# Kernel optimization log

Measured on AMD Instinct MI355X. Metric: run time of the kernel, lower is better.

Reference implementation:

```python
import jax, jax.numpy as jnp
import numpy as np

N, F, E, B, D = 100000, 256, 128, 10000, 32
GAMMA, ZETA = -0.1, 1.1  # hard-concrete stretch params of L0Dense


def setup_inputs() -> dict:
    key = jax.random.key(0)
    ks = jax.random.split(key, 12)
    return {
        "nodes": jax.random.randint(ks[0], (B,), 0, N),
        "neigh_idx": jax.random.randint(ks[1], (B, D), 0, N),
        "neigh_mask": jax.random.bernoulli(ks[2], 0.9, (B, D)),
        "feature": jax.random.normal(ks[3], (N, F), jnp.float32),
        "W": jax.random.normal(ks[4], (F, E), jnp.float32) * 0.05,
        "b": jnp.zeros((E,), jnp.float32),
        "qz_loga": jax.random.normal(ks[5], (F,), jnp.float32),
        "att1_w": jax.random.normal(ks[6], (2 * E, E), jnp.float32) * 0.05,
        "att1_b": jnp.zeros((E,), jnp.float32),
        "att2_w": jax.random.normal(ks[7], (E, E), jnp.float32) * 0.05,
        "att2_b": jnp.zeros((E,), jnp.float32),
        "att3_w": jax.random.normal(ks[8], (E, 1), jnp.float32) * 0.05,
        "att3_b": jnp.zeros((1,), jnp.float32),
    }


def reference(nodes, neigh_idx, neigh_mask, feature, W, b, qz_loga,
              att1_w, att1_b, att2_w, att2_b, att3_w, att3_b):
    # L0Dense, deterministic (eval) hard-concrete gate on input dims
    z = jnp.clip(jax.nn.sigmoid(qz_loga) * (ZETA - GAMMA) + GAMMA, 0.0, 1.0)
    We = W * z[:, None]                                  # [F, E]

    node_feat = feature[nodes] @ We + b                   # [B, E]
    neigh_feat = feature[neigh_idx] @ We + b              # [B, D, E]

    # GraphRec-style attention MLP over (neighbor, center) pairs
    h = jnp.concatenate(
        [neigh_feat, jnp.broadcast_to(node_feat[:, None, :], neigh_feat.shape)],
        axis=-1)                                          # [B, D, 2E]
    h = jax.nn.relu(h @ att1_w + att1_b)
    h = jax.nn.relu(h @ att2_w + att2_b)
    scores = (h @ att3_w + att3_b)[..., 0]                # [B, D]
    scores = jnp.where(neigh_mask, scores, -1e30)
    att = jax.nn.softmax(scores, axis=-1)                 # [B, D]

    agg = jnp.einsum('bd,bde->be', att, neigh_feat)       # weighted sum
    has_neigh = neigh_mask.any(axis=-1, keepdims=True)
    return jnp.where(has_neigh, agg, node_feat)           # n==0 fallback
```

## Files before the change

kernel.cpp:

```cpp
#include <hip/hip_runtime.h>
#include <hip/hip_bf16.h>
#include <math.h>

#define NN 100000
#define FF 256
#define EE 128
#define BB_ 10000
#define DD 32

typedef __attribute__((ext_vector_type(8))) short short8;
typedef __attribute__((ext_vector_type(4))) float f32x4;

__device__ __forceinline__ short f2bf(float f) {
  __hip_bfloat16 h = __float2bfloat16(f);
  union { __hip_bfloat16 h; short s; } u; u.h = h;
  return u.s;
}
__device__ __forceinline__ float bf2f(short s) {
  union { unsigned u; float f; } v;
  v.u = ((unsigned)(unsigned short)s) << 16;
  return v.f;
}

__device__ __forceinline__ void gll16(const float* g, float* lds) {
  __builtin_amdgcn_global_load_lds(
      (const __attribute__((address_space(1))) unsigned int*)g,
      (__attribute__((address_space(3))) unsigned int*)lds, 16, 0, 0);
}

__global__ __launch_bounds__(256) void k_prep(
    const float* __restrict__ W, const float* __restrict__ qz,
    const float* __restrict__ a1w, const float* __restrict__ a2w,
    const float* __restrict__ bb,
    float* __restrict__ Wef32, short* __restrict__ BT2,
    short* __restrict__ a1wTc, short* __restrict__ w2T,
    float* __restrict__ bias2) {
  int i = blockIdx.x * 256 + threadIdx.x;
  if (i < 32768) {
    int f = i >> 7, e = i & 127;
    float g = qz[f];
    float s = 1.0f / (1.0f + expf(-g));
    float z = fminf(fmaxf(s * 1.2f - 0.1f, 0.0f), 1.0f);
    float v = W[f * 128 + e] * z;
    Wef32[f * 128 + e] = v;
    BT2[e * 256 + f] = f2bf(v);
  } else if (i < 49152) {
    int t = i - 32768; int n = t >> 7, k = t & 127;
    a1wTc[n * 128 + k] = f2bf(a1w[(128 + k) * 128 + n]);
  } else if (i < 65536) {
    int t = i - 49152; int n = t >> 7, k = t & 127;
    w2T[n * 128 + k] = f2bf(a2w[k * 128 + n]);
  } else if (i < 65664) {
    bias2[i - 65536] = bb[i - 65536];
  }
}

__global__ __launch_bounds__(256) void k_compose(
    const float* __restrict__ Wef32, const float* __restrict__ a1w,
    const float* __restrict__ a1b, const float* __restrict__ bb,
    short* __restrict__ BT2, float* __restrict__ bias2) {
  const int n = blockIdx.x;
  const int f = threadIdx.x;
  float s = 0.f;
  for (int e = 0; e < 128; ++e)
    s = fmaf(a1w[e * 128 + n], Wef32[f * 128 + e], s);
  BT2[(size_t)(128 + n) * 256 + f] = f2bf(s);
  if (f == 0) {
    float by = a1b[n];
    for (int e = 0; e < 128; ++e) by = fmaf(bb[e], a1w[e * 128 + n], by);
    bias2[128 + n] = by;
  }
}

__global__ __launch_bounds__(256) void k_xy(
    const float* __restrict__ feat, const short* __restrict__ BT2,
    const float* __restrict__ bias2, short* __restrict__ XY, int M) {
  __shared__ float As[2][32 * 256];
  const int tid = threadIdx.x;
  const int wave = tid >> 6, lane = tid & 63;
  const int wn = wave;
  const int l15 = lane & 15, lg = lane >> 4;
  const int NT = M >> 5;
  const int G = gridDim.x;

  short8 bfr[8][4];
#pragma unroll
  for (int ks = 0; ks < 8; ++ks)
#pragma unroll
    for (int j = 0; j < 4; ++j)
      bfr[ks][j] = *(const short8*)(BT2 +
          (size_t)(wn * 64 + j * 16 + l15) * 256 + (ks * 4 + lg) * 8);
  float bv4[4];
#pragma unroll
  for (int j = 0; j < 4; ++j) bv4[j] = bias2[wn * 64 + j * 16 + l15];

  int t = blockIdx.x;
  if (t < NT) {
#pragma unroll
    for (int it = 0; it < 8; ++it) {
      int r = it * 4 + wave;
      gll16(feat + (size_t)(t * 32 + r) * 256 + ((lane ^ (r & 7)) * 4),
            &As[0][r * 256]);
    }
  }

  int cur = 0;
  for (; t < NT; t += G) {
    const int tn = t + G;
    __builtin_amdgcn_s_barrier();
    if (tn < NT) {
#pragma unroll
      for (int it = 0; it < 8; ++it) {
        int r = it * 4 + wave;
        gll16(feat + (size_t)(tn * 32 + r) * 256 + ((lane ^ (r & 7)) * 4),
              &As[cur ^ 1][r * 256]);
      }
      asm volatile("s_waitcnt vmcnt(8)" ::: "memory");
    } else {
      asm volatile("s_waitcnt vmcnt(0)" ::: "memory");
    }
    __builtin_amdgcn_s_barrier();
    __builtin_amdgcn_sched_barrier(0);

    f32x4 acc[2][4];
#pragma unroll
    for (int i = 0; i < 2; ++i)
#pragma unroll
      for (int j = 0; j < 4; ++j) acc[i][j] = (f32x4){0.f, 0.f, 0.f, 0.f};

    const float* Ab = &As[cur][0];
#pragma unroll
    for (int ks = 0; ks < 8; ++ks) {
      const int kg = ks * 4 + lg;
#pragma unroll
      for (int i = 0; i < 2; ++i) {
        const int r = i * 16 + l15;
        const int sw = r & 7;
        const int c0 = (2 * kg) ^ sw;
        const int c1 = (2 * kg + 1) ^ sw;
        float4 flo = *(const float4*)(Ab + r * 256 + c0 * 4);
        float4 fhi = *(const float4*)(Ab + r * 256 + c1 * 4);
        short8 af;
        af[0] = f2bf(flo.x); af[1] = f2bf(flo.y);
        af[2] = f2bf(flo.z); af[3] = f2bf(flo.w);
        af[4] = f2bf(fhi.x); af[5] = f2bf(fhi.y);
        af[6] = f2bf(fhi.z); af[7] = f2bf(fhi.w);
        __builtin_amdgcn_s_setprio(1);
#pragma unroll
        for (int j = 0; j < 4; ++j)
          acc[i][j] = __builtin_amdgcn_mfma_f32_16x16x32_bf16(
              af, bfr[ks][j], acc[i][j], 0, 0, 0);
        __builtin_amdgcn_s_setprio(0);
      }
    }

#pragma unroll
    for (int i = 0; i < 2; ++i) {
#pragma unroll
      for (int r = 0; r < 4; ++r) {
        int row = t * 32 + i * 16 + lg * 4 + r;
#pragma unroll
        for (int j = 0; j < 4; ++j) {
          int col = wn * 64 + j * 16 + l15;
          XY[(size_t)row * 256 + col] = f2bf(acc[i][j][r] + bv4[j]);
        }
      }
    }
    cur ^= 1;
  }
}

template <int K, int LDA, int LDC, bool AF32, bool OUTBF16>
__global__ __launch_bounds__(256) void k_mm(
    const void* __restrict__ Ap, const short* __restrict__ BT,
    const float* __restrict__ bias, const int* __restrict__ idx,
    void* __restrict__ Cp, int M) {
  __shared__ short As[128 * 64];
  __shared__ short Bs[128 * 64];
  const int tid = threadIdx.x;
  const int mb = blockIdx.x * 128;
  const int col0 = blockIdx.y * 128;
  const int wave = tid >> 6, lane = tid & 63;
  const int wr = wave >> 1, wc = wave & 1;
  const int l15 = lane & 15, lg = lane >> 4;

  size_t abase[4];
#pragma unroll
  for (int s = 0; s < 4; ++s) {
    int row = (tid + s * 256) >> 3;
    int grow = mb + row;
    int gr = 0;
    if (grow < M) gr = idx ? idx[grow] : grow;
    abase[s] = (size_t)gr * LDA;
  }

  f32x4 acc[4][4];
#pragma unroll
  for (int i = 0; i < 4; ++i)
#pragma unroll
    for (int j = 0; j < 4; ++j) acc[i][j] = (f32x4){0.f, 0.f, 0.f, 0.f};

  for (int k0 = 0; k0 < K; k0 += 64) {
#pragma unroll
    for (int s = 0; s < 4; ++s) {
      int q = tid + s * 256;
      int row = q >> 3, c = q & 7;
      short8 av;
      if (AF32) {
        const float* ap = (const float*)Ap + abase[s] + k0 + c * 8;
        float4 f0 = *(const float4*)ap;
        float4 f1 = *(const float4*)(ap + 4);
        av[0] = f2bf(f0.x); av[1] = f2bf(f0.y);
        av[2] = f2bf(f0.z); av[3] = f2bf(f0.w);
        av[4] = f2bf(f1.x); av[5] = f2bf(f1.y);
        av[6] = f2bf(f1.z); av[7] = f2bf(f1.w);
      } else {
        av = *(const short8*)((const short*)Ap + abase[s] + k0 + c * 8);
      }
      *(short8*)(As + row * 64 + 8 * (c ^ (row & 7))) = av;
      short8 bv = *(const short8*)(BT + (size_t)(col0 + row) * K + k0 + c * 8);
      *(short8*)(Bs + row * 64 + 8 * (c ^ (row & 7))) = bv;
    }
    __syncthreads();
#pragma unroll
    for (int ks = 0; ks < 2; ++ks) {
      int c = ks * 4 + lg;
      short8 af[4], bfv[4];
#pragma unroll
      for (int i = 0; i < 4; ++i) {
        int r = wr * 64 + i * 16 + l15;
        af[i] = *(short8*)(As + r * 64 + 8 * (c ^ (r & 7)));
        int n = wc * 64 + i * 16 + l15;
        bfv[i] = *(short8*)(Bs + n * 64 + 8 * (c ^ (n & 7)));
      }
#pragma unroll
      for (int i = 0; i < 4; ++i)
#pragma unroll
        for (int j = 0; j < 4; ++j)
          acc[i][j] = __builtin_amdgcn_mfma_f32_16x16x32_bf16(
              af[i], bfv[j], acc[i][j], 0, 0, 0);
    }
    __syncthreads();
  }

  float bv4[4];
#pragma unroll
  for (int j = 0; j < 4; ++j) {
    int col = wc * 64 + j * 16 + l15;
    bv4[j] = bias ? bias[col0 + col] : 0.f;
  }
#pragma unroll
  for (int i = 0; i < 4; ++i) {
#pragma unroll
    for (int r = 0; r < 4; ++r) {
      int row = mb + wr * 64 + i * 16 + lg * 4 + r;
      if (row < M) {
#pragma unroll
        for (int j = 0; j < 4; ++j) {
          int col = wc * 64 + j * 16 + l15;
          float v = acc[i][j][r] + bv4[j];
          if (OUTBF16)
            ((short*)Cp)[(size_t)row * LDC + col0 + col] = f2bf(v);
          else
            ((float*)Cp)[(size_t)row * LDC + col0 + col] = v;
        }
      }
    }
  }
}

__global__ __launch_bounds__(256) void k_attn5(
    const short* __restrict__ XY, const float* __restrict__ P,
    const int* __restrict__ nodes, const int* __restrict__ nidx,
    const int* __restrict__ nmask, const short* __restrict__ w2T,
    const float* __restrict__ b2, const float* __restrict__ w3,
    const float* __restrict__ b3, float* __restrict__ out) {
  __shared__ short xs[4][32 * 128];
  __shared__ float sc_s[4][32];
  __shared__ float att_s[4][32];
  const int tid = threadIdx.x;
  const int wave = tid >> 6, lane = tid & 63;
  const int b = blockIdx.x * 4 + wave;
  const int l15 = lane & 15, lg = lane >> 4;
  const int* nb = nidx + b * DD;

  const int m = nmask[(size_t)b * DD + (lane & 31)];

  short8 xtmp[8];
#pragma unroll
  for (int it = 0; it < 8; ++it)
    xtmp[it] = *(const short8*)(XY + (size_t)nb[it * 4 + lg] * 256 + l15 * 8);
  const int nid0 = nb[l15];
  const int nid1 = nb[16 + l15];
  const short* yr0 = XY + (size_t)nid0 * 256 + 128;
  const short* yr1 = XY + (size_t)nid1 * 256 + 128;
  short8 y0v[4], y1v[4];
#pragma unroll
  for (int ks = 0; ks < 4; ++ks) {
    const int k0 = ks * 32 + lg * 8;
    y0v[ks] = *(const short8*)(yr0 + k0);
    y1v[ks] = *(const short8*)(yr1 + k0);
  }
  const float* pr = P + (size_t)b * EE;
  float4 pv[8];
#pragma unroll
  for (int q = 0; q < 4; ++q) {
    const int k0 = q * 32 + lg * 8;
    pv[2 * q] = *(const float4*)(pr + k0);
    pv[2 * q + 1] = *(const float4*)(pr + k0 + 4);
  }

#pragma unroll
  for (int it = 0; it < 8; ++it)
    *(short8*)&xs[wave][(it * 4 + lg) * 128 + l15 * 8] = xtmp[it];

  short8 a0[4], a1[4];
#pragma unroll
  for (int ks = 0; ks < 4; ++ks) {
    float pf[8] = {pv[2 * ks].x, pv[2 * ks].y, pv[2 * ks].z, pv[2 * ks].w,
                   pv[2 * ks + 1].x, pv[2 * ks + 1].y, pv[2 * ks + 1].z,
                   pv[2 * ks + 1].w};
#pragma unroll
    for (int e = 0; e < 8; ++e) {
      a0[ks][e] = f2bf(fmaxf(bf2f(y0v[ks][e]) + pf[e], 0.f));
      a1[ks][e] = f2bf(fmaxf(bf2f(y1v[ks][e]) + pf[e], 0.f));
    }
  }

  float sp[2][4];
#pragma unroll
  for (int i = 0; i < 2; ++i)
#pragma unroll
    for (int r = 0; r < 4; ++r) sp[i][r] = 0.f;

#pragma unroll
  for (int cg = 0; cg < 2; ++cg) {
    f32x4 acc[2][4];
#pragma unroll
    for (int i = 0; i < 2; ++i)
#pragma unroll
      for (int j = 0; j < 4; ++j) acc[i][j] = (f32x4){0.f, 0.f, 0.f, 0.f};
#pragma unroll
    for (int ks = 0; ks < 4; ++ks) {
      const int k0 = ks * 32 + lg * 8;
      short8 bfv[4];
#pragma unroll
      for (int j = 0; j < 4; ++j)
        bfv[j] = *(const short8*)(w2T +
            (size_t)(cg * 64 + j * 16 + l15) * EE + k0);
      __builtin_amdgcn_s_setprio(1);
#pragma unroll
      for (int j = 0; j < 4; ++j) {
        acc[0][j] = __builtin_amdgcn_mfma_f32_16x16x32_bf16(a0[ks], bfv[j],
                                                            acc[0][j], 0, 0, 0);
        acc[1][j] = __builtin_amdgcn_mfma_f32_16x16x32_bf16(a1[ks], bfv[j],
                                                            acc[1][j], 0, 0, 0);
      }
      __builtin_amdgcn_s_setprio(0);
    }
#pragma unroll
    for (int j = 0; j < 4; ++j) {
      const int col = cg * 64 + j * 16 + l15;
      const float b2v = b2[col];
      const float w3v = w3[col];
#pragma unroll
      for (int i = 0; i < 2; ++i)
#pragma unroll
        for (int r = 0; r < 4; ++r)
          sp[i][r] += fmaxf(acc[i][j][r] + b2v, 0.f) * w3v;
    }
  }

#pragma unroll
  for (int off = 1; off <= 8; off <<= 1) {
#pragma unroll
    for (int i = 0; i < 2; ++i)
#pragma unroll
      for (int r = 0; r < 4; ++r) sp[i][r] += __shfl_xor(sp[i][r], off);
  }
  if (l15 == 0) {
#pragma unroll
    for (int i = 0; i < 2; ++i)
#pragma unroll
      for (int r = 0; r < 4; ++r)
        sc_s[wave][i * 16 + lg * 4 + r] = sp[i][r];
  }

  const int row = lane & 31;
  float s = sc_s[wave][row] + b3[0];
  if (!m) s = -1e30f;
  float mx = s;
#pragma unroll
  for (int off = 1; off <= 16; off <<= 1) mx = fmaxf(mx, __shfl_xor(mx, off));
  float e = expf(s - mx);
  float sum = e;
#pragma unroll
  for (int off = 1; off <= 16; off <<= 1) sum += __shfl_xor(sum, off);
  if (lane < 32) att_s[wave][row] = e / sum;
  const bool has = (__ballot(m != 0) != 0ull);

  float a0f = 0.f, a1f = 0.f;
  if (has) {
#pragma unroll
    for (int d = 0; d < 32; ++d) {
      const float a = att_s[wave][d];
      const unsigned xdw = *(const unsigned*)&xs[wave][d * 128 + 2 * lane];
      a0f += a * bf2f((short)(xdw & 0xffffu));
      a1f += a * bf2f((short)(xdw >> 16));
    }
  } else {
    const short* xr = XY + (size_t)nodes[b] * 256;
    unsigned x2 = *(const unsigned*)(xr + 2 * lane);
    a0f = bf2f((short)(x2 & 0xffffu));
    a1f = bf2f((short)(x2 >> 16));
  }
  *(float2*)(out + (size_t)b * EE + 2 * lane) = make_float2(a0f, a1f);
}

extern "C" void kernel_launch(void* const* d_in, const int* in_sizes, int n_in,
                              void* d_out, int out_size, void* d_ws,
                              size_t ws_size, hipStream_t stream) {
  const int* nodes = (const int*)d_in[0];
  const int* nidx = (const int*)d_in[1];
  const int* nmask = (const int*)d_in[2];
  const float* feature = (const float*)d_in[3];
  const float* W = (const float*)d_in[4];
  const float* bb = (const float*)d_in[5];
  const float* qz = (const float*)d_in[6];
  const float* a1w = (const float*)d_in[7];
  const float* a1b = (const float*)d_in[8];
  const float* a2w = (const float*)d_in[9];
  const float* a2b = (const float*)d_in[10];
  const float* a3w = (const float*)d_in[11];
  const float* a3b = (const float*)d_in[12];
  float* out = (float*)d_out;

  char* ws = (char*)d_ws;
  short* BT2   = (short*)(ws);
  float* Wef32 = (float*)(ws + 131072);
  short* a1wTc = (short*)(ws + 262144);
  short* w2T   = (short*)(ws + 294912);
  float* bias2 = (float*)(ws + 327680);
  short* XYb   = (short*)(ws + 524288);
  float* Pv    = (float*)(ws + 524288 + 51200000);

  k_prep<<<257, 256, 0, stream>>>(W, qz, a1w, a2w, bb, Wef32, BT2, a1wTc, w2T,
                                  bias2);
  k_compose<<<128, 256, 0, stream>>>(Wef32, a1w, a1b, bb, BT2, bias2);
  k_xy<<<512, 256, 0, stream>>>(feature, BT2, bias2, XYb, NN);
  k_mm<128, 256, 128, false, false><<<dim3((BB_ + 127) / 128, 1), 256, 0,
                                      stream>>>(XYb, a1wTc, nullptr, nodes, Pv,
                                                BB_);
  k_attn5<<<BB_ / 4, 256, 0, stream>>>(XYb, Pv, nodes, nidx, nmask, w2T, a2b,
                                       a3w, a3b, out);
}
```

Baseline: 125.0 us.

## Make attention kernel persistent with software-prefetched next batch item

The attention kernel now launches 625 blocks, and each wave processes 4 batch items strided by 2500. Indices, masks, the Y rows and P for the next item are prefetched while the current item's MFMAs run. The X rows for the weighted sum are loaded directly into registers instead of staged through LDS, and b2/w3 are hoisted out of the loop. This aims to hide gather latency, at the cost of higher register pressure (32 extra registers for xv) and fewer blocks to hide latency with.

Measured after the change: 123.0 us. Within noise of the previous version (-1.6%).

```diff
diff --git a/kernel.cpp b/kernel.cpp
--- a/kernel.cpp
+++ b/kernel.cpp
@@ -269,152 +269,178 @@
   }
 }
 
-__global__ __launch_bounds__(256) void k_attn5(
+__global__ __launch_bounds__(256) void k_attn6(
     const short* __restrict__ XY, const float* __restrict__ P,
     const int* __restrict__ nodes, const int* __restrict__ nidx,
     const int* __restrict__ nmask, const short* __restrict__ w2T,
     const float* __restrict__ b2, const float* __restrict__ w3,
     const float* __restrict__ b3, float* __restrict__ out) {
-  __shared__ short xs[4][32 * 128];
   __shared__ float sc_s[4][32];
   __shared__ float att_s[4][32];
   const int tid = threadIdx.x;
   const int wave = tid >> 6, lane = tid & 63;
-  const int b = blockIdx.x * 4 + wave;
   const int l15 = lane & 15, lg = lane >> 4;
-  const int* nb = nidx + b * DD;
-
-  const int m = nmask[(size_t)b * DD + (lane & 31)];
-
-  short8 xtmp[8];
-#pragma unroll
-  for (int it = 0; it < 8; ++it)
-    xtmp[it] = *(const short8*)(XY + (size_t)nb[it * 4 + lg] * 256 + l15 * 8);
-  const int nid0 = nb[l15];
-  const int nid1 = nb[16 + l15];
-  const short* yr0 = XY + (size_t)nid0 * 256 + 128;
-  const short* yr1 = XY + (size_t)nid1 * 256 + 128;
+  const int w0 = blockIdx.x * 4 + wave;
+  const float b3v = b3[0];
+
+  float b2v[2][4], w3v[2][4];
+#pragma unroll
+  for (int cg = 0; cg < 2; ++cg)
+#pragma unroll
+    for (int j = 0; j < 4; ++j) {
+      const int col = cg * 64 + j * 16 + l15;
+      b2v[cg][j] = b2[col];
+      w3v[cg][j] = w3[col];
+    }
+
+  int b = w0;
+  int xc = nidx[b * DD + (lane & 31)];
+  int mc = nmask[b * DD + (lane & 31)];
+  unsigned xfb = *(const unsigned*)(XY + (size_t)nodes[b] * 256 + 2 * lane);
+  int nb0 = __shfl(xc, l15), nb1 = __shfl(xc, 16 + l15);
   short8 y0v[4], y1v[4];
 #pragma unroll
   for (int ks = 0; ks < 4; ++ks) {
     const int k0 = ks * 32 + lg * 8;
-    y0v[ks] = *(const short8*)(yr0 + k0);
-    y1v[ks] = *(const short8*)(yr1 + k0);
-  }
-  const float* pr = P + (size_t)b * EE;
+    y0v[ks] = *(const short8*)(XY + (size_t)nb0 * 256 + 128 + k0);
+    y1v[ks] = *(const short8*)(XY + (size_t)nb1 * 256 + 128 + k0);
+  }
   float4 pv[8];
 #pragma unroll
   for (int q = 0; q < 4; ++q) {
     const int k0 = q * 32 + lg * 8;
-    pv[2 * q] = *(const float4*)(pr + k0);
-    pv[2 * q + 1] = *(const float4*)(pr + k0 + 4);
-  }
-
-#pragma unroll
-  for (int it = 0; it < 8; ++it)
-    *(short8*)&xs[wave][(it * 4 + lg) * 128 + l15 * 8] = xtmp[it];
-
-  short8 a0[4], a1[4];
-#pragma unroll
-  for (int ks = 0; ks < 4; ++ks) {
-    float pf[8] = {pv[2 * ks].x, pv[2 * ks].y, pv[2 * ks].z, pv[2 * ks].w,
-                   pv[2 * ks + 1].x, pv[2 * ks + 1].y, pv[2 * ks + 1].z,
-                   pv[2 * ks + 1].w};
-#pragma unroll
-    for (int e = 0; e < 8; ++e) {
-      a0[ks][e] = f2bf(fmaxf(bf2f(y0v[ks][e]) + pf[e], 0.f));
-      a1[ks][e] = f2bf(fmaxf(bf2f(y1v[ks][e]) + pf[e], 0.f));
-    }
-  }
-
-  float sp[2][4];
-#pragma unroll
-  for (int i = 0; i < 2; ++i)
-#pragma unroll
-    for (int r = 0; r < 4; ++r) sp[i][r] = 0.f;
-
-#pragma unroll
-  for (int cg = 0; cg < 2; ++cg) {
-    f32x4 acc[2][4];
+    pv[2 * q] = *(const float4*)(P + (size_t)b * EE + k0);
+    pv[2 * q + 1] = *(const float4*)(P + (size_t)b * EE + k0 + 4);
+  }
+
+#pragma unroll 1
+  for (int it = 0; it < 4; ++it) {
+    const int bn = (it < 3) ? b + 2500 : b;
+    int xn = nidx[bn * DD + (lane & 31)];
+    int mn = nmask[bn * DD + (lane & 31)];
+    unsigned xfbn =
+        *(const unsigned*)(XY + (size_t)nodes[bn] * 256 + 2 * lane);
+
+    unsigned xv[32];
+#pragma unroll
+    for (int d = 0; d < 32; ++d)
+      xv[d] = *(const unsigned*)(XY + (size_t)__shfl(xc, d) * 256 + 2 * lane);
+
+    short8 a0[4], a1[4];
+#pragma unroll
+    for (int ks = 0; ks < 4; ++ks) {
+      float pf[8] = {pv[2 * ks].x, pv[2 * ks].y, pv[2 * ks].z, pv[2 * ks].w,
+                     pv[2 * ks + 1].x, pv[2 * ks + 1].y, pv[2 * ks + 1].z,
+                     pv[2 * ks + 1].w};
+#pragma unroll
+      for (int e = 0; e < 8; ++e) {
+        a0[ks][e] = f2bf(fmaxf(bf2f(y0v[ks][e]) + pf[e], 0.f));
+        a1[ks][e] = f2bf(fmaxf(bf2f(y1v[ks][e]) + pf[e], 0.f));
+      }
+    }
+
+    float sp[2][4];
 #pragma unroll
     for (int i = 0; i < 2; ++i)
 #pragma unroll
-      for (int j = 0; j < 4; ++j) acc[i][j] = (f32x4){0.f, 0.f, 0.f, 0.f};
-#pragma unroll
-    for (int ks = 0; ks < 4; ++ks) {
-      const int k0 = ks * 32 + lg * 8;
-      short8 bfv[4];
-#pragma unroll
-      for (int j = 0; j < 4; ++j)
-        bfv[j] = *(const short8*)(w2T +
-            (size_t)(cg * 64 + j * 16 + l15) * EE + k0);
-      __builtin_amdgcn_s_setprio(1);
+      for (int r = 0; r < 4; ++r) sp[i][r] = 0.f;
+
+#pragma unroll
+    for (int cg = 0; cg < 2; ++cg) {
+      f32x4 acc[2][4];
+#pragma unroll
+      for (int i = 0; i < 2; ++i)
+#pragma unroll
+        for (int j = 0; j < 4; ++j) acc[i][j] = (f32x4){0.f, 0.f, 0.f, 0.f};
+#pragma unroll
+      for (int ks = 0; ks < 4; ++ks) {
+        const int k0 = ks * 32 + lg * 8;
+        short8 bfv[4];
+#pragma unroll
+        for (int j = 0; j < 4; ++j)
+          bfv[j] = *(const short8*)(w2T +
+              (size_t)(cg * 64 + j * 16 + l15) * EE + k0);
+        __builtin_amdgcn_s_setprio(1);
+#pragma unroll
+        for (int j = 0; j < 4; ++j) {
+          acc[0][j] = __builtin_amdgcn_mfma_f32_16x16x32_bf16(
+              a0[ks], bfv[j], acc[0][j], 0, 0, 0);
+          acc[1][j] = __builtin_amdgcn_mfma_f32_16x16x32_bf16(
+              a1[ks], bfv[j], acc[1][j], 0, 0, 0);
+        }
+        __builtin_amdgcn_s_setprio(0);
+      }
+      if (cg == 0) {
+        const int nb0n = __shfl(xn, l15), nb1n = __shfl(xn, 16 + l15);
+#pragma unroll
+        for (int ks = 0; ks < 4; ++ks) {
+          const int k0 = ks * 32 + lg * 8;
+          y0v[ks] = *(const short8*)(XY + (size_t)nb0n * 256 + 128 + k0);
+          y1v[ks] = *(const short8*)(XY + (size_t)nb1n * 256 + 128 + k0);
+        }
+      }
 #pragma unroll
       for (int j = 0; j < 4; ++j) {
-        acc[0][j] = __builtin_amdgcn_mfma_f32_16x16x32_bf16(a0[ks], bfv[j],
-                                                            acc[0][j], 0, 0, 0);
-        acc[1][j] = __builtin_amdgcn_mfma_f32_16x16x32_bf16(a1[ks], bfv[j],
-                                                            acc[1][j], 0, 0, 0);
-      }
-      __builtin_amdgcn_s_setprio(0);
-    }
-#pragma unroll
-    for (int j = 0; j < 4; ++j) {
-      const int col = cg * 64 + j * 16 + l15;
-      const float b2v = b2[col];
-      const float w3v = w3[col];
+#pragma unroll
+        for (int i = 0; i < 2; ++i)
+#pragma unroll
+          for (int r = 0; r < 4; ++r)
+            sp[i][r] += fmaxf(acc[i][j][r] + b2v[cg][j], 0.f) * w3v[cg][j];
+      }
+    }
+
+#pragma unroll
+    for (int q = 0; q < 4; ++q) {
+      const int k0 = q * 32 + lg * 8;
+      pv[2 * q] = *(const float4*)(P + (size_t)bn * EE + k0);
+      pv[2 * q + 1] = *(const float4*)(P + (size_t)bn * EE + k0 + 4);
+    }
+
+#pragma unroll
+    for (int off = 1; off <= 8; off <<= 1) {
 #pragma unroll
       for (int i = 0; i < 2; ++i)
 #pragma unroll
+        for (int r = 0; r < 4; ++r) sp[i][r] += __shfl_xor(sp[i][r], off);
+    }
+    if (l15 == 0) {
+#pragma unroll
+      for (int i = 0; i < 2; ++i)
+#pragma unroll
         for (int r = 0; r < 4; ++r)
-          sp[i][r] += fmaxf(acc[i][j][r] + b2v, 0.f) * w3v;
-    }
-  }
-
-#pragma unroll
-  for (int off = 1; off <= 8; off <<= 1) {
-#pragma unroll
-    for (int i = 0; i < 2; ++i)
-#pragma unroll
-      for (int r = 0; r < 4; ++r) sp[i][r] += __shfl_xor(sp[i][r], off);
-  }
-  if (l15 == 0) {
-#pragma unroll
-    for (int i = 0; i < 2; ++i)
-#pragma unroll
-      for (int r = 0; r < 4; ++r)
-        sc_s[wave][i * 16 + lg * 4 + r] = sp[i][r];
-  }
-
-  const int row = lane & 31;
-  float s = sc_s[wave][row] + b3[0];
-  if (!m) s = -1e30f;
-  float mx = s;
-#pragma unroll
-  for (int off = 1; off <= 16; off <<= 1) mx = fmaxf(mx, __shfl_xor(mx, off));
-  float e = expf(s - mx);
-  float sum = e;
-#pragma unroll
-  for (int off = 1; off <= 16; off <<= 1) sum += __shfl_xor(sum, off);
-  if (lane < 32) att_s[wave][row] = e / sum;
-  const bool has = (__ballot(m != 0) != 0ull);
-
-  float a0f = 0.f, a1f = 0.f;
-  if (has) {
-#pragma unroll
-    for (int d = 0; d < 32; ++d) {
-      const float a = att_s[wave][d];
-      const unsigned xdw = *(const unsigned*)&xs[wave][d * 128 + 2 * lane];
-      a0f += a * bf2f((short)(xdw & 0xffffu));
-      a1f += a * bf2f((short)(xdw >> 16));
-    }
-  } else {
-    const short* xr = XY + (size_t)nodes[b] * 256;
-    unsigned x2 = *(const unsigned*)(xr + 2 * lane);
-    a0f = bf2f((short)(x2 & 0xffffu));
-    a1f = bf2f((short)(x2 >> 16));
-  }
-  *(float2*)(out + (size_t)b * EE + 2 * lane) = make_float2(a0f, a1f);
+          sc_s[wave][i * 16 + lg * 4 + r] = sp[i][r];
+    }
+
+    const int row = lane & 31;
+    float s = sc_s[wave][row] + b3v;
+    if (!mc) s = -1e30f;
+    float mx = s;
+#pragma unroll
+    for (int off = 1; off <= 16; off <<= 1)
+      mx = fmaxf(mx, __shfl_xor(mx, off));
+    float e = expf(s - mx);
+    float sum = e;
+#pragma unroll
+    for (int off = 1; off <= 16; off <<= 1) sum += __shfl_xor(sum, off);
+    if (lane < 32) att_s[wave][row] = e / sum;
+    const bool has = (__ballot(mc != 0) != 0ull);
+
+    float a0f = 0.f, a1f = 0.f;
+    if (has) {
+#pragma unroll
+      for (int d = 0; d < 32; ++d) {
+        const float a = att_s[wave][d];
+        a0f += a * bf2f((short)(xv[d] & 0xffffu));
+        a1f += a * bf2f((short)(xv[d] >> 16));
+      }
+    } else {
+      a0f = bf2f((short)(xfb & 0xffffu));
+      a1f = bf2f((short)(xfb >> 16));
+    }
+    *(float2*)(out + (size_t)b * EE + 2 * lane) = make_float2(a0f, a1f);
+
+    xc = xn; mc = mn; xfb = xfbn; b = bn;
+  }
 }
 
 extern "C" void kernel_launch(void* const* d_in, const int* in_sizes, int n_in,
@@ -451,6 +477,6 @@
   k_mm<128, 256, 128, false, false><<<dim3((BB_ + 127) / 128, 1), 256, 0,
                                       stream>>>(XYb, a1wTc, nullptr, nodes, Pv,
                                                 BB_);
-  k_attn5<<<BB_ / 4, 256, 0, stream>>>(XYb, Pv, nodes, nidx, nmask, w2T, a2b,
-                                       a3w, a3b, out);
-}
+  k_attn6<<<625, 256, 0, stream>>>(XYb, Pv, nodes, nidx, nmask, w2T, a2b,
+                                   a3w, a3b, out);
+}
```

## Drop precomposed Y projection; compute neighbor attention layer-1 in the attention kernel

Applied to the files above, without the earlier changes.

The node-wide projection used to produce both X and a precomposed Y = X·att1_w_top for all 100k nodes, writing 256 bf16 values per node. Now it writes only X (128 columns), and the attention kernel runs the first attention layer with MFMA on the 32 gathered neighbor rows per center, staging the ReLU output in swizzled LDS. The k_compose launch and the fp32 Wef32 buffer are removed. The aim is to halve the big intermediate write and the gather traffic. The cost is extra MFMA work and LDS traffic inside the attention kernel, with the gathered X rows also held in registers.

After: 135.4 us. +8.3%, slower.

```diff
diff --git a/kernel.cpp b/kernel.cpp
--- a/kernel.cpp
+++ b/kernel.cpp
@@ -31,50 +31,30 @@
 __global__ __launch_bounds__(256) void k_prep(
     const float* __restrict__ W, const float* __restrict__ qz,
     const float* __restrict__ a1w, const float* __restrict__ a2w,
-    const float* __restrict__ bb,
-    float* __restrict__ Wef32, short* __restrict__ BT2,
-    short* __restrict__ a1wTc, short* __restrict__ w2T,
-    float* __restrict__ bias2) {
+    short* __restrict__ BT2, short* __restrict__ a1wTn,
+    short* __restrict__ a1wTc, short* __restrict__ w2T) {
   int i = blockIdx.x * 256 + threadIdx.x;
   if (i < 32768) {
     int f = i >> 7, e = i & 127;
     float g = qz[f];
     float s = 1.0f / (1.0f + expf(-g));
     float z = fminf(fmaxf(s * 1.2f - 0.1f, 0.0f), 1.0f);
-    float v = W[f * 128 + e] * z;
-    Wef32[f * 128 + e] = v;
-    BT2[e * 256 + f] = f2bf(v);
+    BT2[e * 256 + f] = f2bf(W[f * 128 + e] * z);
   } else if (i < 49152) {
-    int t = i - 32768; int n = t >> 7, k = t & 127;
-    a1wTc[n * 128 + k] = f2bf(a1w[(128 + k) * 128 + n]);
+    int t = i - 32768; int c = t >> 7, f = t & 127;
+    a1wTn[c * 128 + f] = f2bf(a1w[f * 128 + c]);
   } else if (i < 65536) {
     int t = i - 49152; int n = t >> 7, k = t & 127;
+    a1wTc[n * 128 + k] = f2bf(a1w[(128 + k) * 128 + n]);
+  } else if (i < 81920) {
+    int t = i - 65536; int n = t >> 7, k = t & 127;
     w2T[n * 128 + k] = f2bf(a2w[k * 128 + n]);
-  } else if (i < 65664) {
-    bias2[i - 65536] = bb[i - 65536];
-  }
-}
-
-__global__ __launch_bounds__(256) void k_compose(
-    const float* __restrict__ Wef32, const float* __restrict__ a1w,
-    const float* __restrict__ a1b, const float* __restrict__ bb,
-    short* __restrict__ BT2, float* __restrict__ bias2) {
-  const int n = blockIdx.x;
-  const int f = threadIdx.x;
-  float s = 0.f;
-  for (int e = 0; e < 128; ++e)
-    s = fmaf(a1w[e * 128 + n], Wef32[f * 128 + e], s);
-  BT2[(size_t)(128 + n) * 256 + f] = f2bf(s);
-  if (f == 0) {
-    float by = a1b[n];
-    for (int e = 0; e < 128; ++e) by = fmaf(bb[e], a1w[e * 128 + n], by);
-    bias2[128 + n] = by;
   }
 }
 
 __global__ __launch_bounds__(256) void k_xy(
     const float* __restrict__ feat, const short* __restrict__ BT2,
-    const float* __restrict__ bias2, short* __restrict__ XY, int M) {
+    const float* __restrict__ bb, short* __restrict__ X, int M) {
   __shared__ float As[2][32 * 256];
   const int tid = threadIdx.x;
   const int wave = tid >> 6, lane = tid & 63;
@@ -83,16 +63,16 @@
   const int NT = M >> 5;
   const int G = gridDim.x;
 
-  short8 bfr[8][4];
+  short8 bfr[8][2];
 #pragma unroll
   for (int ks = 0; ks < 8; ++ks)
 #pragma unroll
-    for (int j = 0; j < 4; ++j)
+    for (int j = 0; j < 2; ++j)
       bfr[ks][j] = *(const short8*)(BT2 +
-          (size_t)(wn * 64 + j * 16 + l15) * 256 + (ks * 4 + lg) * 8);
-  float bv4[4];
-#pragma unroll
-  for (int j = 0; j < 4; ++j) bv4[j] = bias2[wn * 64 + j * 16 + l15];
+          (size_t)(wn * 32 + j * 16 + l15) * 256 + (ks * 4 + lg) * 8);
+  float bv2[2];
+#pragma unroll
+  for (int j = 0; j < 2; ++j) bv2[j] = bb[wn * 32 + j * 16 + l15];
 
   int t = blockIdx.x;
   if (t < NT) {
@@ -122,11 +102,11 @@
     __builtin_amdgcn_s_barrier();
     __builtin_amdgcn_sched_barrier(0);
 
-    f32x4 acc[2][4];
+    f32x4 acc[2][2];
 #pragma unroll
     for (int i = 0; i < 2; ++i)
 #pragma unroll
-      for (int j = 0; j < 4; ++j) acc[i][j] = (f32x4){0.f, 0.f, 0.f, 0.f};
+      for (int j = 0; j < 2; ++j) acc[i][j] = (f32x4){0.f, 0.f, 0.f, 0.f};
 
     const float* Ab = &As[cur][0];
 #pragma unroll
@@ -147,7 +127,7 @@
         af[6] = f2bf(fhi.z); af[7] = f2bf(fhi.w);
         __builtin_amdgcn_s_setprio(1);
 #pragma unroll
-        for (int j = 0; j < 4; ++j)
+        for (int j = 0; j < 2; ++j)
           acc[i][j] = __builtin_amdgcn_mfma_f32_16x16x32_bf16(
               af, bfr[ks][j], acc[i][j], 0, 0, 0);
         __builtin_amdgcn_s_setprio(0);
@@ -160,9 +140,9 @@
       for (int r = 0; r < 4; ++r) {
         int row = t * 32 + i * 16 + lg * 4 + r;
 #pragma unroll
-        for (int j = 0; j < 4; ++j) {
-          int col = wn * 64 + j * 16 + l15;
-          XY[(size_t)row * 256 + col] = f2bf(acc[i][j][r] + bv4[j]);
+        for (int j = 0; j < 2; ++j) {
+          int col = wn * 32 + j * 16 + l15;
+          X[(size_t)row * EE + col] = f2bf(acc[i][j][r] + bv2[j]);
         }
       }
     }
@@ -170,16 +150,14 @@
   }
 }
 
-template <int K, int LDA, int LDC, bool AF32, bool OUTBF16>
 __global__ __launch_bounds__(256) void k_mm(
-    const void* __restrict__ Ap, const short* __restrict__ BT,
+    const short* __restrict__ Ap, const short* __restrict__ BT,
     const float* __restrict__ bias, const int* __restrict__ idx,
-    void* __restrict__ Cp, int M) {
+    float* __restrict__ Cp, int M) {
   __shared__ short As[128 * 64];
   __shared__ short Bs[128 * 64];
   const int tid = threadIdx.x;
   const int mb = blockIdx.x * 128;
-  const int col0 = blockIdx.y * 128;
   const int wave = tid >> 6, lane = tid & 63;
   const int wr = wave >> 1, wc = wave & 1;
   const int l15 = lane & 15, lg = lane >> 4;
@@ -190,8 +168,8 @@
     int row = (tid + s * 256) >> 3;
     int grow = mb + row;
     int gr = 0;
-    if (grow < M) gr = idx ? idx[grow] : grow;
-    abase[s] = (size_t)gr * LDA;
+    if (grow < M) gr = idx[grow];
+    abase[s] = (size_t)gr * EE;
   }
 
   f32x4 acc[4][4];
@@ -200,25 +178,14 @@
 #pragma unroll
     for (int j = 0; j < 4; ++j) acc[i][j] = (f32x4){0.f, 0.f, 0.f, 0.f};
 
-  for (int k0 = 0; k0 < K; k0 += 64) {
+  for (int k0 = 0; k0 < 128; k0 += 64) {
 #pragma unroll
     for (int s = 0; s < 4; ++s) {
       int q = tid + s * 256;
       int row = q >> 3, c = q & 7;
-      short8 av;
-      if (AF32) {
-        const float* ap = (const float*)Ap + abase[s] + k0 + c * 8;
-        float4 f0 = *(const float4*)ap;
-        float4 f1 = *(const float4*)(ap + 4);
-        av[0] = f2bf(f0.x); av[1] = f2bf(f0.y);
-        av[2] = f2bf(f0.z); av[3] = f2bf(f0.w);
-        av[4] = f2bf(f1.x); av[5] = f2bf(f1.y);
-        av[6] = f2bf(f1.z); av[7] = f2bf(f1.w);
-      } else {
-        av = *(const short8*)((const short*)Ap + abase[s] + k0 + c * 8);
-      }
+      short8 av = *(const short8*)(Ap + abase[s] + k0 + c * 8);
       *(short8*)(As + row * 64 + 8 * (c ^ (row & 7))) = av;
-      short8 bv = *(const short8*)(BT + (size_t)(col0 + row) * K + k0 + c * 8);
+      short8 bv = *(const short8*)(BT + (size_t)row * 128 + k0 + c * 8);
       *(short8*)(Bs + row * 64 + 8 * (c ^ (row & 7))) = bv;
     }
     __syncthreads();
@@ -245,10 +212,7 @@
 
   float bv4[4];
 #pragma unroll
-  for (int j = 0; j < 4; ++j) {
-    int col = wc * 64 + j * 16 + l15;
-    bv4[j] = bias ? bias[col0 + col] : 0.f;
-  }
+  for (int j = 0; j < 4; ++j) bv4[j] = bias[wc * 64 + j * 16 + l15];
 #pragma unroll
   for (int i = 0; i < 4; ++i) {
 #pragma unroll
@@ -258,91 +222,108 @@
 #pragma unroll
         for (int j = 0; j < 4; ++j) {
           int col = wc * 64 + j * 16 + l15;
-          float v = acc[i][j][r] + bv4[j];
-          if (OUTBF16)
-            ((short*)Cp)[(size_t)row * LDC + col0 + col] = f2bf(v);
-          else
-            ((float*)Cp)[(size_t)row * LDC + col0 + col] = v;
+          Cp[(size_t)row * EE + col] = acc[i][j][r] + bv4[j];
         }
       }
     }
   }
 }
 
-__global__ __launch_bounds__(256) void k_attn5(
-    const short* __restrict__ XY, const float* __restrict__ P,
+__global__ __launch_bounds__(256) void k_attn9(
+    const short* __restrict__ Xb, const float* __restrict__ P,
     const int* __restrict__ nodes, const int* __restrict__ nidx,
-    const int* __restrict__ nmask, const short* __restrict__ w2T,
-    const float* __restrict__ b2, const float* __restrict__ w3,
-    const float* __restrict__ b3, float* __restrict__ out) {
-  __shared__ short xs[4][32 * 128];
+    const int* __restrict__ nmask, const short* __restrict__ a1nT,
+    const short* __restrict__ w2T, const float* __restrict__ b2,
+    const float* __restrict__ w3, const float* __restrict__ b3,
+    float* __restrict__ out) {
+  __shared__ short h1s[4][32 * 128];
   __shared__ float sc_s[4][32];
   __shared__ float att_s[4][32];
   const int tid = threadIdx.x;
   const int wave = tid >> 6, lane = tid & 63;
+  const int l15 = lane & 15, lg = lane >> 4;
+  const int dl = lane & 31;
   const int b = blockIdx.x * 4 + wave;
-  const int l15 = lane & 15, lg = lane >> 4;
-  const int* nb = nidx + b * DD;
-
-  const int m = nmask[(size_t)b * DD + (lane & 31)];
-
-  short8 xtmp[8];
-#pragma unroll
-  for (int it = 0; it < 8; ++it)
-    xtmp[it] = *(const short8*)(XY + (size_t)nb[it * 4 + lg] * 256 + l15 * 8);
-  const int nid0 = nb[l15];
-  const int nid1 = nb[16 + l15];
-  const short* yr0 = XY + (size_t)nid0 * 256 + 128;
-  const short* yr1 = XY + (size_t)nid1 * 256 + 128;
-  short8 y0v[4], y1v[4];
+
+  const int ni = nidx[b * DD + dl];
+  const int m = nmask[b * DD + dl];
+  const int r0 = __shfl(ni, l15);
+  const int r1 = __shfl(ni, 16 + l15);
+
+  short8 xa0[4], xa1[4];
 #pragma unroll
   for (int ks = 0; ks < 4; ++ks) {
     const int k0 = ks * 32 + lg * 8;
-    y0v[ks] = *(const short8*)(yr0 + k0);
-    y1v[ks] = *(const short8*)(yr1 + k0);
-  }
-  const float* pr = P + (size_t)b * EE;
-  float4 pv[8];
-#pragma unroll
-  for (int q = 0; q < 4; ++q) {
-    const int k0 = q * 32 + lg * 8;
-    pv[2 * q] = *(const float4*)(pr + k0);
-    pv[2 * q + 1] = *(const float4*)(pr + k0 + 4);
-  }
-
-#pragma unroll
-  for (int it = 0; it < 8; ++it)
-    *(short8*)&xs[wave][(it * 4 + lg) * 128 + l15 * 8] = xtmp[it];
-
-  short8 a0[4], a1[4];
-#pragma unroll
-  for (int ks = 0; ks < 4; ++ks) {
-    float pf[8] = {pv[2 * ks].x, pv[2 * ks].y, pv[2 * ks].z, pv[2 * ks].w,
-                   pv[2 * ks + 1].x, pv[2 * ks + 1].y, pv[2 * ks + 1].z,
-                   pv[2 * ks + 1].w};
-#pragma unroll
-    for (int e = 0; e < 8; ++e) {
-      a0[ks][e] = f2bf(fmaxf(bf2f(y0v[ks][e]) + pf[e], 0.f));
-      a1[ks][e] = f2bf(fmaxf(bf2f(y1v[ks][e]) + pf[e], 0.f));
-    }
-  }
-
-  float sp[2][4];
-#pragma unroll
-  for (int i = 0; i < 2; ++i)
-#pragma unroll
-    for (int r = 0; r < 4; ++r) sp[i][r] = 0.f;
+    xa0[ks] = *(const short8*)(Xb + (size_t)r0 * EE + k0);
+    xa1[ks] = *(const short8*)(Xb + (size_t)r1 * EE + k0);
+  }
+  unsigned xv[32];
+#pragma unroll
+  for (int d = 0; d < 32; ++d)
+    xv[d] = *(const unsigned*)(Xb + (size_t)__shfl(ni, d) * EE + 2 * lane);
 
 #pragma unroll
   for (int cg = 0; cg < 2; ++cg) {
-    f32x4 acc[2][4];
+    f32x4 a1[2][4];
 #pragma unroll
     for (int i = 0; i < 2; ++i)
 #pragma unroll
-      for (int j = 0; j < 4; ++j) acc[i][j] = (f32x4){0.f, 0.f, 0.f, 0.f};
+      for (int j = 0; j < 4; ++j) a1[i][j] = (f32x4){0.f, 0.f, 0.f, 0.f};
 #pragma unroll
     for (int ks = 0; ks < 4; ++ks) {
       const int k0 = ks * 32 + lg * 8;
+      short8 bfv[4];
+#pragma unroll
+      for (int j = 0; j < 4; ++j)
+        bfv[j] = *(const short8*)(a1nT +
+            (size_t)(cg * 64 + j * 16 + l15) * EE + k0);
+      __builtin_amdgcn_s_setprio(1);
+#pragma unroll
+      for (int j = 0; j < 4; ++j) {
+        a1[0][j] = __builtin_amdgcn_mfma_f32_16x16x32_bf16(xa0[ks], bfv[j],
+                                                           a1[0][j], 0, 0, 0);
+        a1[1][j] = __builtin_amdgcn_mfma_f32_16x16x32_bf16(xa1[ks], bfv[j],
+                                                           a1[1][j], 0, 0, 0);
+      }
+      __builtin_amdgcn_s_setprio(0);
+    }
+#pragma unroll
+    for (int j = 0; j < 4; ++j) {
+      const int col = cg * 64 + j * 16 + l15;
+      const float pj = P[(size_t)b * EE + col];
+      const int cc = col >> 3;
+      const int ce = col & 7;
+#pragma unroll
+      for (int i = 0; i < 2; ++i)
+#pragma unroll
+        for (int r = 0; r < 4; ++r) {
+          const int row = i * 16 + lg * 4 + r;
+          h1s[wave][row * 128 + 8 * (cc ^ (row & 7)) + ce] =
+              f2bf(fmaxf(a1[i][j][r] + pj, 0.f));
+        }
+    }
+  }
+
+  float sp[2][4];
+#pragma unroll
+  for (int i = 0; i < 2; ++i)
+#pragma unroll
+    for (int r = 0; r < 4; ++r) sp[i][r] = 0.f;
+
+#pragma unroll
+  for (int cg = 0; cg < 2; ++cg) {
+    f32x4 a2[2][4];
+#pragma unroll
+    for (int i = 0; i < 2; ++i)
+#pragma unroll
+      for (int j = 0; j < 4; ++j) a2[i][j] = (f32x4){0.f, 0.f, 0.f, 0.f};
+#pragma unroll
+    for (int ks = 0; ks < 4; ++ks) {
+      const int k0 = ks * 32 + lg * 8;
+      const int c = ks * 4 + lg;
+      short8 af0 = *(short8*)&h1s[wave][l15 * 128 + 8 * (c ^ (l15 & 7))];
+      short8 af1 =
+          *(short8*)&h1s[wave][(16 + l15) * 128 + 8 * (c ^ (l15 & 7))];
       short8 bfv[4];
 #pragma unroll
       for (int j = 0; j < 4; ++j)
@@ -351,10 +332,10 @@
       __builtin_amdgcn_s_setprio(1);
 #pragma unroll
       for (int j = 0; j < 4; ++j) {
-        acc[0][j] = __builtin_amdgcn_mfma_f32_16x16x32_bf16(a0[ks], bfv[j],
-                                                            acc[0][j], 0, 0, 0);
-        acc[1][j] = __builtin_amdgcn_mfma_f32_16x16x32_bf16(a1[ks], bfv[j],
-                                                            acc[1][j], 0, 0, 0);
+        a2[0][j] = __builtin_amdgcn_mfma_f32_16x16x32_bf16(af0, bfv[j],
+                                                           a2[0][j], 0, 0, 0);
+        a2[1][j] = __builtin_amdgcn_mfma_f32_16x16x32_bf16(af1, bfv[j],
+                                                           a2[1][j], 0, 0, 0);
       }
       __builtin_amdgcn_s_setprio(0);
     }
@@ -367,7 +348,7 @@
       for (int i = 0; i < 2; ++i)
 #pragma unroll
         for (int r = 0; r < 4; ++r)
-          sp[i][r] += fmaxf(acc[i][j][r] + b2v, 0.f) * w3v;
+          sp[i][r] += fmaxf(a2[i][j][r] + b2v, 0.f) * w3v;
     }
   }
 
@@ -386,8 +367,7 @@
         sc_s[wave][i * 16 + lg * 4 + r] = sp[i][r];
   }
 
-  const int row = lane & 31;
-  float s = sc_s[wave][row] + b3[0];
+  float s = sc_s[wave][dl] + b3[0];
   if (!m) s = -1e30f;
   float mx = s;
 #pragma unroll
@@ -396,7 +376,7 @@
   float sum = e;
 #pragma unroll
   for (int off = 1; off <= 16; off <<= 1) sum += __shfl_xor(sum, off);
-  if (lane < 32) att_s[wave][row] = e / sum;
+  if (lane < 32) att_s[wave][dl] = e / sum;
   const bool has = (__ballot(m != 0) != 0ull);
 
   float a0f = 0.f, a1f = 0.f;
@@ -404,15 +384,14 @@
 #pragma unroll
     for (int d = 0; d < 32; ++d) {
       const float a = att_s[wave][d];
-      const unsigned xdw = *(const unsigned*)&xs[wave][d * 128 + 2 * lane];
-      a0f += a * bf2f((short)(xdw & 0xffffu));
-      a1f += a * bf2f((short)(xdw >> 16));
+      a0f += a * bf2f((short)(xv[d] & 0xffffu));
+      a1f += a * bf2f((short)(xv[d] >> 16));
     }
   } else {
-    const short* xr = XY + (size_t)nodes[b] * 256;
-    unsigned x2 = *(const unsigned*)(xr + 2 * lane);
-    a0f = bf2f((short)(x2 & 0xffffu));
-    a1f = bf2f((short)(x2 >> 16));
+    const unsigned xfb =
+        *(const unsigned*)(Xb + (size_t)nodes[b] * EE + 2 * lane);
+    a0f = bf2f((short)(xfb & 0xffffu));
+    a1f = bf2f((short)(xfb >> 16));
   }
   *(float2*)(out + (size_t)b * EE + 2 * lane) = make_float2(a0f, a1f);
 }
@@ -437,20 +416,15 @@
 
   char* ws = (char*)d_ws;
   short* BT2   = (short*)(ws);
-  float* Wef32 = (float*)(ws + 131072);
-  short* a1wTc = (short*)(ws + 262144);
-  short* w2T   = (short*)(ws + 294912);
-  float* bias2 = (float*)(ws + 327680);
-  short* XYb   = (short*)(ws + 524288);
-  float* Pv    = (float*)(ws + 524288 + 51200000);
-
-  k_prep<<<257, 256, 0, stream>>>(W, qz, a1w, a2w, bb, Wef32, BT2, a1wTc, w2T,
-                                  bias2);
-  k_compose<<<128, 256, 0, stream>>>(Wef32, a1w, a1b, bb, BT2, bias2);
-  k_xy<<<512, 256, 0, stream>>>(feature, BT2, bias2, XYb, NN);
-  k_mm<128, 256, 128, false, false><<<dim3((BB_ + 127) / 128, 1), 256, 0,
-                                      stream>>>(XYb, a1wTc, nullptr, nodes, Pv,
-                                                BB_);
-  k_attn5<<<BB_ / 4, 256, 0, stream>>>(XYb, Pv, nodes, nidx, nmask, w2T, a2b,
-                                       a3w, a3b, out);
-}
+  short* a1nT  = (short*)(ws + 65536);
+  short* a1wTc = (short*)(ws + 98304);
+  short* w2T   = (short*)(ws + 131072);
+  short* Xb    = (short*)(ws + 262144);
+  float* Pv    = (float*)(ws + 262144 + 25600000);
+
+  k_prep<<<320, 256, 0, stream>>>(W, qz, a1w, a2w, BT2, a1nT, a1wTc, w2T);
+  k_xy<<<512, 256, 0, stream>>>(feature, BT2, bb, Xb, NN);
+  k_mm<<<(BB_ + 127) / 128, 256, 0, stream>>>(Xb, a1wTc, a1b, nodes, Pv, BB_);
+  k_attn9<<<BB_ / 4, 256, 0, stream>>>(Xb, Pv, nodes, nidx, nmask, a1nT, w2T,
+                                       a2b, a3w, a3b, out);
+}
```
